# Kernel tuning notes

Measured on AMD Instinct MI355X. Metric: run time of the kernel, lower is better.

The kernel has to match this reference:

```python
import jax, jax.numpy as jnp
import numpy as np
import math

EMBED_DIM = 1024
NUM_HEADS = 16
HEAD_DIM = EMBED_DIM // NUM_HEADS
BATCH = 2
SEQ = 2048
GATE_EPS = 1e-4


def setup_inputs() -> dict:
    key = jax.random.key(0)
    ks = jax.random.split(key, 6)
    scale_e = 1.0 / math.sqrt(EMBED_DIM)
    scale_h = 1.0 / math.sqrt(HEAD_DIM)
    return {
        "hidden_states": jax.random.normal(ks[0], (BATCH, SEQ, EMBED_DIM), dtype=jnp.float32),
        "attention_mask": jnp.zeros((BATCH, 1, 1, SEQ), dtype=jnp.float32),
        "W_q": jax.random.normal(ks[1], (NUM_HEADS, EMBED_DIM, HEAD_DIM), dtype=jnp.float32) * scale_e,
        "W_k": jax.random.normal(ks[2], (NUM_HEADS, EMBED_DIM, HEAD_DIM), dtype=jnp.float32) * scale_e,
        "W_v": jax.random.normal(ks[3], (NUM_HEADS, EMBED_DIM, HEAD_DIM), dtype=jnp.float32) * scale_e,
        "W_o": jax.random.normal(ks[4], (NUM_HEADS, HEAD_DIM, EMBED_DIM), dtype=jnp.float32) * scale_h,
        "gate": jnp.ones((NUM_HEADS,), dtype=jnp.float32),
    }


def reference(hidden_states, attention_mask, W_q, W_k, W_v, W_o, gate):
    # Effective gate: heads with gate < 1e-4 are skipped (contribute zero).
    eff_gate = jnp.where(gate >= GATE_EPS, gate, 0.0)  # [H]

    # Batched per-head projections: x [B,S,E], W [H,E,D] -> [B,H,S,D]
    q = jnp.einsum("bse,hed->bhsd", hidden_states, W_q)
    k = jnp.einsum("bse,hed->bhsd", hidden_states, W_k)
    v = jnp.einsum("bse,hed->bhsd", hidden_states, W_v)

    scores = jnp.einsum("bhsd,bhtd->bhst", q, k) / math.sqrt(HEAD_DIM)
    scores = scores + attention_mask  # [B,1,1,S] broadcasts over heads/queries
    probs = jax.nn.softmax(scores, axis=-1)

    context = jnp.einsum("bhst,bhtd->bhsd", probs, v)
    head_out = jnp.einsum("bhsd,hde->bhse", context, W_o)

    out = jnp.einsum("h,bhse->bse", eff_gate, head_out)

    # Final rescale: divide by max(1, active_gates / num_heads) when any head active.
    active = jnp.sum((gate > GATE_EPS).astype(jnp.float32))
    denom = jnp.maximum(1.0, active / NUM_HEADS)
    out = jnp.where(active > 0, out / denom, out)
    return out
```

## Files before the change

kernel.cpp:

```cpp
#include <hip/hip_runtime.h>
#include <hip/hip_bf16.h>

typedef short bf16x4 __attribute__((ext_vector_type(4)));
typedef short bf16x8 __attribute__((ext_vector_type(8)));
typedef float f32x4  __attribute__((ext_vector_type(4)));

#define LOG2E 1.4426950408889634f
#define QSCALE (0.125f * LOG2E)

__device__ __forceinline__ short f2bf(float x) {
  union { __hip_bfloat16 h; short s; } u;
  u.h = __float2bfloat16(x);
  return u.s;
}

__device__ __forceinline__ float fast_exp2(float x) {
#if __has_builtin(__builtin_amdgcn_exp2f)
  return __builtin_amdgcn_exp2f(x);
#else
  return exp2f(x);
#endif
}

__device__ __forceinline__ void load16_lds(const void* g, void* l) {
#if __has_builtin(__builtin_amdgcn_global_load_lds)
  __builtin_amdgcn_global_load_lds(
      (const __attribute__((address_space(1))) unsigned int*)g,
      (__attribute__((address_space(3))) unsigned int*)l, 16, 0, 0);
#else
  const int lane = threadIdx.x & 63;
  *(bf16x8*)((char*)l + lane * 16) = *(const bf16x8*)((const char*)g + lane * 16);
#endif
}

__global__ void gate_kernel(const float* __restrict__ gate, float* __restrict__ scale) {
  const int h = threadIdx.x;
  if (h >= 16) return;
  const float g = gate[h];
  const float eff = (g >= 1e-4f) ? g : 0.f;
  int active = 0;
  for (int j = 0; j < 16; ++j) active += (gate[j] > 1e-4f) ? 1 : 0;
  const float denom = fmaxf(1.f, (float)active / 16.f);
  scale[h] = eff / denom;
}

__global__ __launch_bounds__(256)
void cvt_x_kernel(const float* __restrict__ in, short* __restrict__ out, int n4) {
  for (int i = blockIdx.x * blockDim.x + threadIdx.x; i < n4; i += gridDim.x * blockDim.x) {
    const float4 v = ((const float4*)in)[i];
    bf16x4 o;
    o[0] = f2bf(v.x); o[1] = f2bf(v.y); o[2] = f2bf(v.z); o[3] = f2bf(v.w);
    ((bf16x4*)out)[i] = o;
  }
}

__global__ __launch_bounds__(256)
void trans_all_kernel(const float* __restrict__ Wq, const float* __restrict__ Wk,
                      const float* __restrict__ Wv, const float* __restrict__ Wo,
                      short* __restrict__ Wt3, short* __restrict__ Wot) {
  __shared__ float t[32][33];
  const int f = blockIdx.x;
  const float* in;
  short* out;
  int R, C, r0, c0;
  if (f < 3072) {
    const int which = f >> 10;
    const int rem = f & 1023;
    const int z = rem >> 6;
    const int xy = rem & 63;
    in = (which == 0 ? Wq : which == 1 ? Wk : Wv) + (size_t)z * 65536;
    out = Wt3 + (size_t)which * 1048576 + (size_t)z * 65536;
    R = 1024; C = 64; r0 = (xy >> 1) * 32; c0 = (xy & 1) * 32;
  } else {
    const int rem = f - 3072;
    in = Wo; out = Wot;
    R = 1024; C = 1024; r0 = (rem >> 5) * 32; c0 = (rem & 31) * 32;
  }
  const int tr = threadIdx.x >> 5, tc = threadIdx.x & 31;
#pragma unroll
  for (int p = 0; p < 4; ++p)
    t[tr + p * 8][tc] = in[(size_t)(r0 + tr + p * 8) * C + c0 + tc];
  __syncthreads();
#pragma unroll
  for (int p = 0; p < 4; ++p)
    out[(size_t)(c0 + tr + p * 8) * R + r0 + tc] = f2bf(t[tc][tr + p * 8]);
}

__global__ __launch_bounds__(256)
void gemm_qkv_kernel(const short* __restrict__ A, const short* __restrict__ Bt,
                     short* __restrict__ Qb, short* __restrict__ Kb,
                     short* __restrict__ Vt) {
  __shared__ short Al[128 * 32];
  __shared__ short Bl[128 * 32];
  const int tid = threadIdx.x;
  const int w = tid >> 6, lane = tid & 63;
  const int lq = lane & 15, lg = lane >> 4;
  const int m0 = blockIdx.x * 128, n0 = blockIdx.y * 128;
  const int which = n0 >> 10;
  const int wr = (w >> 1) * 64, wc = (w & 1) * 64;

  f32x4 acc[4][4] = {};
  const int grow = lane >> 2;
  const int gcol = (lane & 3) * 8;

  for (int k0 = 0; k0 < 1024; k0 += 32) {
#pragma unroll
    for (int c = 0; c < 2; ++c) {
      const int chunk = (w << 1) | c;
      const int row = chunk * 16 + grow;
      load16_lds(A + (size_t)(m0 + row) * 1024 + k0 + gcol, &Al[chunk * 512]);
      load16_lds(Bt + (size_t)(n0 + row) * 1024 + k0 + gcol, &Bl[chunk * 512]);
    }
    __syncthreads();
    bf16x8 af[4], bfr[4];
#pragma unroll
    for (int i = 0; i < 4; ++i)
      af[i] = *(const bf16x8*)&Al[(wr + i * 16 + lq) * 32 + lg * 8];
#pragma unroll
    for (int j = 0; j < 4; ++j)
      bfr[j] = *(const bf16x8*)&Bl[(wc + j * 16 + lq) * 32 + lg * 8];
#pragma unroll
    for (int i = 0; i < 4; ++i)
#pragma unroll
      for (int j = 0; j < 4; ++j)
        acc[i][j] = __builtin_amdgcn_mfma_f32_16x16x32_bf16(af[i], bfr[j], acc[i][j], 0, 0, 0);
    __syncthreads();
  }

  if (which < 2) {
    short* Out = which ? Kb : Qb;
    const float sc = which ? 1.f : QSCALE;
#pragma unroll
    for (int i = 0; i < 4; ++i)
#pragma unroll
      for (int j = 0; j < 4; ++j) {
        const int nn = (n0 + wc + j * 16 + lq) & 1023;
        const int h = nn >> 6, d = nn & 63;
#pragma unroll
        for (int r = 0; r < 4; ++r) {
          const int m = m0 + wr + i * 16 + lg * 4 + r;
          const int b = m >> 11, s = m & 2047;
          Out[(size_t)((b * 16 + h) * 2048 + s) * 64 + d] = f2bf(acc[i][j][r] * sc);
        }
      }
  } else {
#pragma unroll
    for (int i = 0; i < 4; ++i) {
      const int mb = m0 + wr + i * 16 + lg * 4;
      const int b = mb >> 11, s = mb & 2047;
#pragma unroll
      for (int j = 0; j < 4; ++j) {
        const int nn = (n0 + wc + j * 16 + lq) & 1023;
        const int h = nn >> 6, d = nn & 63;
        bf16x4 o;
#pragma unroll
        for (int r = 0; r < 4; ++r) o[r] = f2bf(acc[i][j][r]);
        *(bf16x4*)&Vt[(size_t)((b * 16 + h) * 64 + d) * 2048 + s] = o;
      }
    }
  }
}

__global__ __launch_bounds__(256)
void gemm_out_kernel(const short* __restrict__ A, const short* __restrict__ Bt,
                     float* __restrict__ Out) {
  __shared__ short Al[128 * 32];
  __shared__ short Bl[128 * 32];
  const int tid = threadIdx.x;
  const int w = tid >> 6, lane = tid & 63;
  const int lq = lane & 15, lg = lane >> 4;
  const int m0 = blockIdx.x * 128, n0 = blockIdx.y * 128;
  const int wr = (w >> 1) * 64, wc = (w & 1) * 64;

  f32x4 acc[4][4] = {};
  const int grow = lane >> 2;
  const int gcol = (lane & 3) * 8;

  for (int k0 = 0; k0 < 1024; k0 += 32) {
#pragma unroll
    for (int c = 0; c < 2; ++c) {
      const int chunk = (w << 1) | c;
      const int row = chunk * 16 + grow;
      load16_lds(A + (size_t)(m0 + row) * 1024 + k0 + gcol, &Al[chunk * 512]);
      load16_lds(Bt + (size_t)(n0 + row) * 1024 + k0 + gcol, &Bl[chunk * 512]);
    }
    __syncthreads();
    bf16x8 af[4], bfr[4];
#pragma unroll
    for (int i = 0; i < 4; ++i)
      af[i] = *(const bf16x8*)&Al[(wr + i * 16 + lq) * 32 + lg * 8];
#pragma unroll
    for (int j = 0; j < 4; ++j)
      bfr[j] = *(const bf16x8*)&Bl[(wc + j * 16 + lq) * 32 + lg * 8];
#pragma unroll
    for (int i = 0; i < 4; ++i)
#pragma unroll
      for (int j = 0; j < 4; ++j)
        acc[i][j] = __builtin_amdgcn_mfma_f32_16x16x32_bf16(af[i], bfr[j], acc[i][j], 0, 0, 0);
    __syncthreads();
  }

#pragma unroll
  for (int i = 0; i < 4; ++i)
#pragma unroll
    for (int r = 0; r < 4; ++r) {
      const int m = m0 + wr + i * 16 + lg * 4 + r;
      float* orow = Out + (size_t)m * 1024 + n0 + wc;
#pragma unroll
      for (int j = 0; j < 4; ++j) orow[j * 16 + lq] = acc[i][j][r];
    }
}

__global__ __launch_bounds__(256, 2)
void attn_kernel(const short* __restrict__ Qb, const short* __restrict__ Kb,
                 const short* __restrict__ Vt, const float* __restrict__ mask,
                 const float* __restrict__ gscale, short* __restrict__ ctx) {
  __shared__ __align__(16) char lds[66560];

  const int tid = threadIdx.x;
  const int w = tid >> 6, lane = tid & 63;
  const int lq = lane & 15, lg = lane >> 4;
  const int bh = blockIdx.y, b = bh >> 4, h = bh & 15;
  const int q0 = blockIdx.x * 64;
  const size_t bhoff = (size_t)bh * 2048 * 64;

  bf16x8 qf[4][2];
#pragma unroll
  for (int qt = 0; qt < 4; ++qt) {
    const short* qp = Qb + bhoff + (size_t)(q0 + qt * 16 + lq) * 64 + lg * 8;
    qf[qt][0] = *(const bf16x8*)qp;
    qf[qt][1] = *(const bf16x8*)(qp + 32);
  }

  const int koffs = (lane >> 3) * 128 + (((lane & 7) * 16) ^ ((lane >> 3) << 4));
  const int vrowc = lane >> 4;
  const int vs_e = ((lane & 15) * 16) ^ (vrowc << 4);
  const int vs_o = ((lane & 15) * 16) ^ ((vrowc + 4) << 4);
  const char* KbB = (const char*)(Kb + bhoff);
  const char* VtB = (const char*)(Vt + bhoff);

  const int sw = (lq & 7) << 4;
  const int kcol0 = (lg * 16) ^ sw, kcol1 = (64 + lg * 16) ^ sw;
  const int vcol0 = (w * 64 + lg * 8) ^ sw, vcol1 = (w * 64 + 32 + lg * 8) ^ sw;
  const float* maskp = mask + b * 2048;

  f32x4 acc[4][4] = {};
  f32x4 lacc[4] = {};

#define STAGE(T, P)                                                              \
  {                                                                              \
    char* kd = lds + (P)*16384 + w * 4096;                                       \
    const char* ks = KbB + (size_t)((T)*128 + w * 32) * 128 + koffs;             \
    char* vd = lds + 32768 + (P)*16384 + w * 4096;                               \
    const char* vsb = VtB + (size_t)(w * 16 + vrowc) * 4096 + (T)*256;           \
    load16_lds(ks, kd);                                                          \
    load16_lds(ks + 1024, kd + 1024);                                            \
    load16_lds(ks + 2048, kd + 2048);                                            \
    load16_lds(ks + 3072, kd + 3072);                                            \
    load16_lds(vsb + vs_e, vd);                                                  \
    load16_lds(vsb + 16384 + vs_o, vd + 1024);                                   \
    load16_lds(vsb + 32768 + vs_e, vd + 2048);                                   \
    load16_lds(vsb + 49152 + vs_o, vd + 3072);                                   \
  }

  STAGE(0, 0);
  __syncthreads();

  for (int t = 0; t < 16; ++t) {
    const int cur = t & 1;
    const f32x4 mk0 = *(const f32x4*)(maskp + t * 128 + w * 32 + lg * 4);
    const f32x4 mk1 = *(const f32x4*)(maskp + t * 128 + w * 32 + 16 + lg * 4);
    if (t < 15) STAGE(t + 1, cur ^ 1);

    const char* Kc = lds + cur * 16384 + (w * 32 + lq) * 128;
    f32x4 s[2][4];
#pragma unroll
    for (int kt = 0; kt < 2; ++kt) {
      const bf16x8 ka0 = *(const bf16x8*)(Kc + kt * 2048 + kcol0);
      const bf16x8 ka1 = *(const bf16x8*)(Kc + kt * 2048 + kcol1);
#pragma unroll
      for (int qt = 0; qt < 4; ++qt) {
        f32x4 ts = {};
        ts = __builtin_amdgcn_mfma_f32_16x16x32_bf16(ka0, qf[qt][0], ts, 0, 0, 0);
        ts = __builtin_amdgcn_mfma_f32_16x16x32_bf16(ka1, qf[qt][1], ts, 0, 0, 0);
        s[kt][qt] = ts;
      }
    }

    bf16x4 pf[2][4];
#pragma unroll
    for (int kt = 0; kt < 2; ++kt) {
      const f32x4 mkv = kt ? mk1 : mk0;
#pragma unroll
      for (int qt = 0; qt < 4; ++qt) {
        const float p0 = fast_exp2(fmaf(mkv[0], LOG2E, s[kt][qt][0]));
        const float p1 = fast_exp2(fmaf(mkv[1], LOG2E, s[kt][qt][1]));
        const float p2 = fast_exp2(fmaf(mkv[2], LOG2E, s[kt][qt][2]));
        const float p3 = fast_exp2(fmaf(mkv[3], LOG2E, s[kt][qt][3]));
        pf[kt][qt][0] = f2bf(p0); pf[kt][qt][1] = f2bf(p1);
        pf[kt][qt][2] = f2bf(p2); pf[kt][qt][3] = f2bf(p3);
        const f32x4 pv = {p0, p1, p2, p3};
        lacc[qt] += pv;
      }
    }

    bf16x8 pb[4];
#pragma unroll
    for (int qt = 0; qt < 4; ++qt)
      pb[qt] = __builtin_shufflevector(pf[0][qt], pf[1][qt], 0, 1, 2, 3, 4, 5, 6, 7);
#pragma unroll
    for (int dt = 0; dt < 4; ++dt) {
      const char* Vrow = lds + 32768 + cur * 16384 + (dt * 16 + lq) * 256;
      const bf16x4 v0 = *(const bf16x4*)(Vrow + vcol0);
      const bf16x4 v1 = *(const bf16x4*)(Vrow + vcol1);
      const bf16x8 av = __builtin_shufflevector(v0, v1, 0, 1, 2, 3, 4, 5, 6, 7);
#pragma unroll
      for (int qt = 0; qt < 4; ++qt)
        acc[dt][qt] = __builtin_amdgcn_mfma_f32_16x16x32_bf16(av, pb[qt], acc[dt][qt], 0, 0, 0);
    }

    __syncthreads();
  }
#undef STAGE

#pragma unroll
  for (int dt = 0; dt < 4; ++dt)
#pragma unroll
    for (int qt = 0; qt < 4; ++qt)
      *(f32x4*)(lds + w * 16384 + (qt * 16 + lq) * 256 + ((dt * 64 + lg * 16) ^ sw)) =
          acc[dt][qt];

  float* Lb = (float*)(lds + 65536);
#pragma unroll
  for (int qt = 0; qt < 4; ++qt) {
    float lt = (lacc[qt][0] + lacc[qt][1]) + (lacc[qt][2] + lacc[qt][3]);
    lt += __shfl_xor(lt, 16);
    lt += __shfl_xor(lt, 32);
    if (lg == 0) Lb[w * 64 + qt * 16 + lq] = lt;
  }
  __syncthreads();

  const float lsum = Lb[w * 16 + lq] + Lb[64 + w * 16 + lq] +
                     Lb[128 + w * 16 + lq] + Lb[192 + w * 16 + lq];
  const float osc = gscale[h] / lsum;
  const int qabs = q0 + w * 16 + lq;
#pragma unroll
  for (int dt = 0; dt < 4; ++dt) {
    const int dby = (dt * 64 + lg * 16) ^ sw;
    f32x4 o = *(const f32x4*)(lds + (w * 16 + lq) * 256 + dby);
    o += *(const f32x4*)(lds + 16384 + (w * 16 + lq) * 256 + dby);
    o += *(const f32x4*)(lds + 32768 + (w * 16 + lq) * 256 + dby);
    o += *(const f32x4*)(lds + 49152 + (w * 16 + lq) * 256 + dby);
    bf16x4 ob;
#pragma unroll
    for (int r = 0; r < 4; ++r) ob[r] = f2bf(o[r] * osc);
    *(bf16x4*)&ctx[(size_t)(b * 2048 + qabs) * 1024 + h * 64 + dt * 16 + lg * 4] = ob;
  }
}

extern "C" void kernel_launch(void* const* d_in, const int* in_sizes, int n_in,
                              void* d_out, int out_size, void* d_ws, size_t ws_size,
                              hipStream_t stream) {
  (void)in_sizes; (void)n_in; (void)out_size; (void)ws_size;
  const float* x    = (const float*)d_in[0];
  const float* mask = (const float*)d_in[1];
  const float* Wq   = (const float*)d_in[2];
  const float* Wk   = (const float*)d_in[3];
  const float* Wv   = (const float*)d_in[4];
  const float* Wo   = (const float*)d_in[5];
  const float* gate = (const float*)d_in[6];
  float* out = (float*)d_out;

  char* ws = (char*)d_ws;
  const size_t MB = 1024 * 1024;
  float* scale = (float*)ws;
  short* Xb  = (short*)(ws + 256);
  short* Wt3 = (short*)(ws + 256 + 8 * MB);
  short* Wot = (short*)(ws + 256 + 14 * MB);
  short* Qb  = (short*)(ws + 256 + 16 * MB);
  short* Kb  = (short*)(ws + 256 + 24 * MB);
  short* Vt  = (short*)(ws + 256 + 32 * MB);
  short* ctx = (short*)(ws + 256 + 40 * MB);

  gate_kernel<<<1, 64, 0, stream>>>(gate, scale);
  cvt_x_kernel<<<2048, 256, 0, stream>>>(x, Xb, 4194304 / 4);
  trans_all_kernel<<<4096, 256, 0, stream>>>(Wq, Wk, Wv, Wo, Wt3, Wot);
  gemm_qkv_kernel<<<dim3(32, 24), 256, 0, stream>>>(Xb, Wt3, Qb, Kb, Vt);
  attn_kernel<<<dim3(32, 32), 256, 0, stream>>>(Qb, Kb, Vt, mask, scale, ctx);
  gemm_out_kernel<<<dim3(32, 8), 256, 0, stream>>>(ctx, Wot, out);
}
```

Baseline: 198.4 us.

## Fold gate kernel into attention, vectorize QK stores, remap attention grid, halve out-GEMM tile

Removes the separate gate kernel launch and computes the per-head gate scale inside the attention kernel. In the QKV GEMM the MFMA operands are swapped for Q/K so each lane holds four consecutive head-dim values, which turns the scalar bf16 stores into bf16x4 vector stores. The attention grid becomes 1D with a remapping that interleaves batch-heads across consecutive blocks, likely to spread load across XCDs and L2. The output GEMM tile drops from 128x128 to 64x128, doubling the block count to 512 for better CU occupancy, at the cost of reloading more B data.

```diff
diff --git a/kernel.cpp b/kernel.cpp
--- a/kernel.cpp
+++ b/kernel.cpp
@@ -31,17 +31,6 @@
   const int lane = threadIdx.x & 63;
   *(bf16x8*)((char*)l + lane * 16) = *(const bf16x8*)((const char*)g + lane * 16);
 #endif
-}
-
-__global__ void gate_kernel(const float* __restrict__ gate, float* __restrict__ scale) {
-  const int h = threadIdx.x;
-  if (h >= 16) return;
-  const float g = gate[h];
-  const float eff = (g >= 1e-4f) ? g : 0.f;
-  int active = 0;
-  for (int j = 0; j < 16; ++j) active += (gate[j] > 1e-4f) ? 1 : 0;
-  const float denom = fmaxf(1.f, (float)active / 16.f);
-  scale[h] = eff / denom;
 }
 
 __global__ __launch_bounds__(256)
@@ -119,30 +108,40 @@
 #pragma unroll
     for (int j = 0; j < 4; ++j)
       bfr[j] = *(const bf16x8*)&Bl[(wc + j * 16 + lq) * 32 + lg * 8];
-#pragma unroll
-    for (int i = 0; i < 4; ++i)
-#pragma unroll
-      for (int j = 0; j < 4; ++j)
-        acc[i][j] = __builtin_amdgcn_mfma_f32_16x16x32_bf16(af[i], bfr[j], acc[i][j], 0, 0, 0);
+    if (which < 2) {
+#pragma unroll
+      for (int i = 0; i < 4; ++i)
+#pragma unroll
+        for (int j = 0; j < 4; ++j)
+          acc[i][j] = __builtin_amdgcn_mfma_f32_16x16x32_bf16(bfr[j], af[i], acc[i][j], 0, 0, 0);
+    } else {
+#pragma unroll
+      for (int i = 0; i < 4; ++i)
+#pragma unroll
+        for (int j = 0; j < 4; ++j)
+          acc[i][j] = __builtin_amdgcn_mfma_f32_16x16x32_bf16(af[i], bfr[j], acc[i][j], 0, 0, 0);
+    }
     __syncthreads();
   }
 
   if (which < 2) {
     short* Out = which ? Kb : Qb;
     const float sc = which ? 1.f : QSCALE;
-#pragma unroll
-    for (int i = 0; i < 4; ++i)
+    const int m = m0 + wr + lq;
+#pragma unroll
+    for (int i = 0; i < 4; ++i) {
+      const int mm = m + i * 16;
+      const int b = mm >> 11, s = mm & 2047;
 #pragma unroll
       for (int j = 0; j < 4; ++j) {
-        const int nn = (n0 + wc + j * 16 + lq) & 1023;
+        const int nn = (n0 + wc + j * 16 + lg * 4) & 1023;
         const int h = nn >> 6, d = nn & 63;
-#pragma unroll
-        for (int r = 0; r < 4; ++r) {
-          const int m = m0 + wr + i * 16 + lg * 4 + r;
-          const int b = m >> 11, s = m & 2047;
-          Out[(size_t)((b * 16 + h) * 2048 + s) * 64 + d] = f2bf(acc[i][j][r] * sc);
-        }
+        bf16x4 o;
+#pragma unroll
+        for (int r = 0; r < 4; ++r) o[r] = f2bf(acc[i][j][r] * sc);
+        *(bf16x4*)&Out[(size_t)((b * 16 + h) * 2048 + s) * 64 + d] = o;
       }
+    }
   } else {
 #pragma unroll
     for (int i = 0; i < 4; ++i) {
@@ -164,36 +163,39 @@
 __global__ __launch_bounds__(256)
 void gemm_out_kernel(const short* __restrict__ A, const short* __restrict__ Bt,
                      float* __restrict__ Out) {
-  __shared__ short Al[128 * 32];
+  __shared__ short Al[64 * 32];
   __shared__ short Bl[128 * 32];
   const int tid = threadIdx.x;
   const int w = tid >> 6, lane = tid & 63;
   const int lq = lane & 15, lg = lane >> 4;
-  const int m0 = blockIdx.x * 128, n0 = blockIdx.y * 128;
-  const int wr = (w >> 1) * 64, wc = (w & 1) * 64;
-
-  f32x4 acc[4][4] = {};
+  const int m0 = blockIdx.x * 64, n0 = blockIdx.y * 128;
+  const int wr = (w >> 1) * 32, wc = (w & 1) * 64;
+
+  f32x4 acc[2][4] = {};
   const int grow = lane >> 2;
   const int gcol = (lane & 3) * 8;
 
   for (int k0 = 0; k0 < 1024; k0 += 32) {
-#pragma unroll
-    for (int c = 0; c < 2; ++c) {
-      const int chunk = (w << 1) | c;
-      const int row = chunk * 16 + grow;
-      load16_lds(A + (size_t)(m0 + row) * 1024 + k0 + gcol, &Al[chunk * 512]);
-      load16_lds(Bt + (size_t)(n0 + row) * 1024 + k0 + gcol, &Bl[chunk * 512]);
+    {
+      const int arow = w * 16 + grow;
+      load16_lds(A + (size_t)(m0 + arow) * 1024 + k0 + gcol, &Al[w * 512]);
+#pragma unroll
+      for (int c = 0; c < 2; ++c) {
+        const int chunk = (w << 1) | c;
+        const int row = chunk * 16 + grow;
+        load16_lds(Bt + (size_t)(n0 + row) * 1024 + k0 + gcol, &Bl[chunk * 512]);
+      }
     }
     __syncthreads();
-    bf16x8 af[4], bfr[4];
-#pragma unroll
-    for (int i = 0; i < 4; ++i)
+    bf16x8 af[2], bfr[4];
+#pragma unroll
+    for (int i = 0; i < 2; ++i)
       af[i] = *(const bf16x8*)&Al[(wr + i * 16 + lq) * 32 + lg * 8];
 #pragma unroll
     for (int j = 0; j < 4; ++j)
       bfr[j] = *(const bf16x8*)&Bl[(wc + j * 16 + lq) * 32 + lg * 8];
 #pragma unroll
-    for (int i = 0; i < 4; ++i)
+    for (int i = 0; i < 2; ++i)
 #pragma unroll
       for (int j = 0; j < 4; ++j)
         acc[i][j] = __builtin_amdgcn_mfma_f32_16x16x32_bf16(af[i], bfr[j], acc[i][j], 0, 0, 0);
@@ -201,7 +203,7 @@
   }
 
 #pragma unroll
-  for (int i = 0; i < 4; ++i)
+  for (int i = 0; i < 2; ++i)
 #pragma unroll
     for (int r = 0; r < 4; ++r) {
       const int m = m0 + wr + i * 16 + lg * 4 + r;
@@ -214,15 +216,24 @@
 __global__ __launch_bounds__(256, 2)
 void attn_kernel(const short* __restrict__ Qb, const short* __restrict__ Kb,
                  const short* __restrict__ Vt, const float* __restrict__ mask,
-                 const float* __restrict__ gscale, short* __restrict__ ctx) {
+                 const float* __restrict__ gate, short* __restrict__ ctx) {
   __shared__ __align__(16) char lds[66560];
 
   const int tid = threadIdx.x;
   const int w = tid >> 6, lane = tid & 63;
   const int lq = lane & 15, lg = lane >> 4;
-  const int bh = blockIdx.y, b = bh >> 4, h = bh & 15;
-  const int q0 = blockIdx.x * 64;
+  const int l = blockIdx.x;
+  const int bh = (l & 7) * 4 + (l >> 8);
+  const int q0 = ((l >> 3) & 31) * 64;
+  const int b = bh >> 4, h = bh & 15;
   const size_t bhoff = (size_t)bh * 2048 * 64;
+
+  const float g = gate[h];
+  const float eff = (g >= 1e-4f) ? g : 0.f;
+  int active = 0;
+#pragma unroll
+  for (int j = 0; j < 16; ++j) active += (gate[j] > 1e-4f) ? 1 : 0;
+  const float gsc = eff / fmaxf(1.f, (float)active / 16.f);
 
   bf16x8 qf[4][2];
 #pragma unroll
@@ -342,7 +353,7 @@
 
   const float lsum = Lb[w * 16 + lq] + Lb[64 + w * 16 + lq] +
                      Lb[128 + w * 16 + lq] + Lb[192 + w * 16 + lq];
-  const float osc = gscale[h] / lsum;
+  const float osc = gsc / lsum;
   const int qabs = q0 + w * 16 + lq;
 #pragma unroll
   for (int dt = 0; dt < 4; ++dt) {
@@ -373,7 +384,6 @@
 
   char* ws = (char*)d_ws;
   const size_t MB = 1024 * 1024;
-  float* scale = (float*)ws;
   short* Xb  = (short*)(ws + 256);
   short* Wt3 = (short*)(ws + 256 + 8 * MB);
   short* Wot = (short*)(ws + 256 + 14 * MB);
@@ -382,10 +392,9 @@
   short* Vt  = (short*)(ws + 256 + 32 * MB);
   short* ctx = (short*)(ws + 256 + 40 * MB);
 
-  gate_kernel<<<1, 64, 0, stream>>>(gate, scale);
   cvt_x_kernel<<<2048, 256, 0, stream>>>(x, Xb, 4194304 / 4);
   trans_all_kernel<<<4096, 256, 0, stream>>>(Wq, Wk, Wv, Wo, Wt3, Wot);
   gemm_qkv_kernel<<<dim3(32, 24), 256, 0, stream>>>(Xb, Wt3, Qb, Kb, Vt);
-  attn_kernel<<<dim3(32, 32), 256, 0, stream>>>(Qb, Kb, Vt, mask, scale, ctx);
-  gemm_out_kernel<<<dim3(32, 8), 256, 0, stream>>>(ctx, Wot, out);
-}
+  attn_kernel<<<1024, 256, 0, stream>>>(Qb, Kb, Vt, mask, gate, ctx);
+  gemm_out_kernel<<<dim3(64, 8), 256, 0, stream>>>(ctx, Wot, out);
+}
```

New measurement: 206.3 us. +4.0%, slower.
